# Kernel tuning notes

Hardware: AMD Instinct MI355X
Metric: run time of the kernel (lower is better)

The kernel has to match this reference:

```python
import jax, jax.numpy as jnp
import numpy as np


def setup_inputs() -> dict:
    key = jax.random.key(0)
    k1, k2 = jax.random.split(key)
    latent = jax.random.normal(k1, (131072, 128), dtype=jnp.float32)
    coords = jax.random.normal(k2, (2048, 128), dtype=jnp.float32)
    return {"latent": latent, "coords": coords}


def reference(latent, coords):
    # torch.cdist(latent, coords).min(1)[1]
    # argmin over euclidean distance == argmin over squared distance,
    # so we skip the sqrt (same result, cheaper and numerically safer).
    x2 = jnp.sum(latent * latent, axis=1, keepdims=True)          # [N, 1]
    c2 = jnp.sum(coords * coords, axis=1)                          # [C]
    cross = latent @ coords.T                                      # [N, C]
    d2 = x2 + c2[None, :] - 2.0 * cross                            # [N, C] squared dists
    return jnp.argmin(d2, axis=1)                                  # [N] int indices
```

## Files before the change

kernel.cpp:

```cpp
#include <hip/hip_runtime.h>


constexpr int D = 128;
constexpr int C = 2048;
constexpr int NCH = 32;
constexpr int NCHUNKS = C / NCH;
constexpr int WL_CAP = 32768;

constexpr size_t WS_CNT = 16384;
constexpr size_t WS_WL  = 32768;
constexpr size_t WS_C2F = 196608;
constexpr size_t WS_BH  = 262144;
constexpr size_t WS_BL  = 524288;

typedef __attribute__((ext_vector_type(4))) int i32x4;
typedef unsigned int u32;

__device__ __forceinline__ int pack4(int a0, int a1, int a2, int a3) {
    return (int)(((u32)a0 & 255u) | (((u32)a1 & 255u) << 8) |
                 (((u32)a2 & 255u) << 16) | (((u32)a3 & 255u) << 24));
}

__device__ __forceinline__ void q2(float v, float qa, float inv, float inv128,
                                   int* h, int* l) {
    float hf = __builtin_rintf(v * inv);
    *h = (int)hf;
    float r = fmaf(-hf, qa, v);
    *l = (int)__builtin_rintf(r * inv128);
}

__device__ __forceinline__ void gl_lds16(const void* g, void* l) {
    __builtin_amdgcn_global_load_lds(
        (const __attribute__((address_space(1))) u32*)g,
        (__attribute__((address_space(3))) u32*)l, 16, 0, 0);
}

__global__ __launch_bounds__(1024) void prep_coords(
        const float* __restrict__ coords,
        signed char* __restrict__ Bh,
        signed char* __restrict__ Bl,
        float* __restrict__ c2f, float* __restrict__ qBout,
        int* __restrict__ counter) {
    __shared__ float sW[16];
    int t = blockIdx.x * blockDim.x + threadIdx.x;
    if (t == 0) *counter = 0;

    float m = 0.f;
    for (int i = threadIdx.x; i < C * D / 4; i += 1024) {
        float4 v = ((const float4*)coords)[i];
        m = fmaxf(m, fmaxf(fmaxf(fabsf(v.x), fabsf(v.y)),
                           fmaxf(fabsf(v.z), fabsf(v.w))));
    }
#pragma unroll
    for (int s = 1; s <= 32; s <<= 1) m = fmaxf(m, __shfl_xor(m, s, 64));
    if ((threadIdx.x & 63) == 0) sW[threadIdx.x >> 6] = m;
    __syncthreads();
    float aB = 1e-30f;
#pragma unroll
    for (int i = 0; i < 16; ++i) aB = fmaxf(aB, sW[i]);

    float qb = aB * (1.f / 127.f);
    float inv = 127.f / aB;
    float inv128 = inv * 128.f;
    if (t == 0) *qBout = qb;

    int c = t >> 2, p = t & 3;
    float v[32];
#pragma unroll
    for (int i = 0; i < 8; ++i)
        *(float4*)(v + i * 4) = *(const float4*)(coords + (size_t)c * D + p * 32 + i * 4);
    float ss = 0.f;
#pragma unroll
    for (int j = 0; j < 32; ++j) ss = fmaf(v[j], v[j], ss);
#pragma unroll
    for (int s = 1; s <= 2; s <<= 1) ss += __shfl_xor(ss, s, 64);

#pragma unroll
    for (int g = 0; g < 2; ++g) {
        int g8 = p * 2 + g;
        int hw[4], lw[4];
#pragma unroll
        for (int w = 0; w < 4; ++w) {
            int h0, l0, h1, l1, h2, l2, h3, l3;
            q2(v[g * 16 + w * 4 + 0], qb, inv, inv128, &h0, &l0);
            q2(v[g * 16 + w * 4 + 1], qb, inv, inv128, &h1, &l1);
            q2(v[g * 16 + w * 4 + 2], qb, inv, inv128, &h2, &l2);
            q2(v[g * 16 + w * 4 + 3], qb, inv, inv128, &h3, &l3);
            hw[w] = pack4(h0, h1, h2, h3);
            lw[w] = pack4(l0, l1, l2, l3);
        }
        size_t off = (size_t)c * 128 + (size_t)((g8 ^ (c & 7)) * 16);
        *(i32x4*)(Bh + off) = (i32x4){hw[0], hw[1], hw[2], hw[3]};
        *(i32x4*)(Bl + off) = (i32x4){lw[0], lw[1], lw[2], lw[3]};
    }
    if (p == 0) c2f[c] = -64.f * ss / qb;
}


__global__ __launch_bounds__(256, 2) void centroid_fast(
        const float* __restrict__ latent,
        const signed char* __restrict__ Bh_img,
        const signed char* __restrict__ Bl_img,
        const float* __restrict__ c2f,
        const float* __restrict__ qBp,
        int* __restrict__ out,
        int* __restrict__ counter,
        int* __restrict__ worklist) {
    __shared__ __align__(16) signed char Bh[2][NCH * 128], Bl[2][NCH * 128];

    const int tid  = threadIdx.x;
    const int wid  = tid >> 6;
    const int lane = tid & 63;
    const int q    = lane >> 4, lr = lane & 15;
    const int row_block = blockIdx.x * 128;

    {
        int ph = (blockIdx.x ^ (blockIdx.x >> 8)) & 3;
        for (int i = 0; i < ph * 2; ++i) __builtin_amdgcn_s_sleep(8);
    }

    gl_lds16(Bh_img + tid * 16, &Bh[0][tid * 16]);
    gl_lds16(Bl_img + tid * 16, &Bl[0][tid * 16]);

    const float qB = *qBp;

    i32x4 Ah[2][2], Al[2][2];
    float invqA, qa;
    {
        float v[2][32];
#pragma unroll
        for (int mt = 0; mt < 2; ++mt) {
            const float* rp = latent + (size_t)(row_block + wid * 32 + mt * 16 + lr) * D;
#pragma unroll
            for (int ks = 0; ks < 2; ++ks)
#pragma unroll
                for (int i = 0; i < 4; ++i)
                    *(float4*)(v[mt] + ks * 16 + i * 4) =
                        *(const float4*)(rp + ks * 64 + q * 16 + i * 4);
        }
        float amax = 0.f;
#pragma unroll
        for (int mt = 0; mt < 2; ++mt)
#pragma unroll
            for (int j = 0; j < 32; ++j) amax = fmaxf(amax, fabsf(v[mt][j]));
#pragma unroll
        for (int s = 1; s <= 32; s <<= 1) amax = fmaxf(amax, __shfl_xor(amax, s, 64));
        amax = fmaxf(amax, 1e-30f);
        qa = amax * (1.f / 127.f);
        invqA = 1.f / qa;
        float inv = 127.f / amax;
        float inv128 = inv * 128.f;
#pragma unroll
        for (int mt = 0; mt < 2; ++mt)
#pragma unroll
            for (int ks = 0; ks < 2; ++ks) {
                int hw[4], lw[4];
#pragma unroll
                for (int w = 0; w < 4; ++w) {
                    int h0, l0, h1, l1, h2, l2, h3, l3;
                    q2(v[mt][ks * 16 + w * 4 + 0], qa, inv, inv128, &h0, &l0);
                    q2(v[mt][ks * 16 + w * 4 + 1], qa, inv, inv128, &h1, &l1);
                    q2(v[mt][ks * 16 + w * 4 + 2], qa, inv, inv128, &h2, &l2);
                    q2(v[mt][ks * 16 + w * 4 + 3], qa, inv, inv128, &h3, &l3);
                    hw[w] = pack4(h0, h1, h2, h3);
                    lw[w] = pack4(l0, l1, l2, l3);
                }
                Ah[mt][ks] = (i32x4){hw[0], hw[1], hw[2], hw[3]};
                Al[mt][ks] = (i32x4){lw[0], lw[1], lw[2], lw[3]};
            }
    }
    const int M_int = (int)(1.28f / (qa * qB)) + 1;

    int b1[8], b2[8], bidx[8];
#pragma unroll
    for (int s = 0; s < 8; ++s) {
        b1[s] = -2147483647 - 1; b2[s] = -2147483647 - 1; bidx[s] = 0;
    }

    __syncthreads();

    for (int ch = 0; ch < NCHUNKS; ++ch) {
        const int buf = ch & 1;
        const int chbase = ch * NCH;
        if (ch + 1 < NCHUNKS) {
            const signed char* sh = Bh_img + (size_t)(ch + 1) * (NCH * 128);
            const signed char* sl = Bl_img + (size_t)(ch + 1) * (NCH * 128);
            gl_lds16(sh + tid * 16, &Bh[buf ^ 1][tid * 16]);
            gl_lds16(sl + tid * 16, &Bl[buf ^ 1][tid * 16]);
            asm volatile("s_waitcnt vmcnt(2)" ::: "memory");
        } else {
            asm volatile("s_waitcnt vmcnt(0)" ::: "memory");
        }
        __builtin_amdgcn_s_barrier();

        float cf[2];
        cf[0] = c2f[chbase + lr];
        cf[1] = c2f[chbase + 16 + lr];

#pragma unroll
        for (int nt = 0; nt < 2; ++nt) {
            const int nl = nt * 16 + lr;
            const int v0 = (int)__builtin_rintf(cf[nt] * invqA);
            i32x4 I1[2], I2[2];
#pragma unroll
            for (int mt = 0; mt < 2; ++mt) {
                I1[mt] = (i32x4){0, 0, 0, 0};
                I2[mt] = (i32x4){v0, v0, v0, v0};
            }
            __builtin_amdgcn_s_setprio(1);
#pragma unroll
            for (int ks = 0; ks < 2; ++ks) {
                const int e = nl * 128 + (((ks << 2) | q) ^ (lr & 7)) * 16;
                i32x4 bh = *(const i32x4*)(&Bh[buf][e]);
                i32x4 bl = *(const i32x4*)(&Bl[buf][e]);
#pragma unroll
                for (int mt = 0; mt < 2; ++mt)
                    I1[mt] = __builtin_amdgcn_mfma_i32_16x16x64_i8(Ah[mt][ks], bh, I1[mt], 0, 0, 0);
#pragma unroll
                for (int mt = 0; mt < 2; ++mt)
                    I2[mt] = __builtin_amdgcn_mfma_i32_16x16x64_i8(Ah[mt][ks], bl, I2[mt], 0, 0, 0);
#pragma unroll
                for (int mt = 0; mt < 2; ++mt)
                    I2[mt] = __builtin_amdgcn_mfma_i32_16x16x64_i8(Al[mt][ks], bh, I2[mt], 0, 0, 0);
            }
            __builtin_amdgcn_s_setprio(0);
            const int n_global = chbase + nl;
#pragma unroll
            for (int mt = 0; mt < 2; ++mt)
#pragma unroll
                for (int r = 0; r < 4; ++r) {
                    int slot = mt * 4 + r;
                    int S = (int)(((u32)I1[mt][r] << 7) + (u32)I2[mt][r]);
                    bool gt  = S > b1[slot];
                    b2[slot]   = max(b2[slot], min(S, b1[slot]));
                    b1[slot]   = max(S, b1[slot]);
                    bidx[slot] = gt ? n_global : bidx[slot];
                }
        }
        __builtin_amdgcn_s_barrier();
    }

#pragma unroll
    for (int m = 1; m <= 8; m <<= 1) {
#pragma unroll
        for (int s = 0; s < 8; ++s) {
            int oa = __shfl_xor(b1[s], m, 64);
            int ob = __shfl_xor(b2[s], m, 64);
            int oi = __shfl_xor(bidx[s], m, 64);
            int mn = min(b1[s], oa);
            b2[s] = max(max(b2[s], ob), mn);
            bool take = oa > b1[s];
            b1[s]   = take ? oa : b1[s];
            bidx[s] = take ? oi : bidx[s];
        }
    }
#pragma unroll
    for (int s = 0; s < 8; ++s) {
        if (lr == s) {
            int row = row_block + wid * 32 + (s >> 2) * 16 + q * 4 + (s & 3);
            out[row] = bidx[s];
            if (b1[s] - b2[s] < M_int) {
                int w = atomicAdd(counter, 1);
                if (w < WL_CAP) worklist[w] = row;
            }
        }
    }
}


__global__ __launch_bounds__(1024) void refine_fp64(
        const float* __restrict__ latent, const float* __restrict__ coords,
        const int* __restrict__ worklist, const int* __restrict__ counter,
        int wl_cap, int* __restrict__ out) {
    __shared__ float  xs[D];
    __shared__ double rv[1024];
    __shared__ int    ri[1024];

    int n = *counter;
    if (n > wl_cap) n = wl_cap;

    for (int wi = blockIdx.x; wi < n; wi += gridDim.x) {
        int row = worklist[wi];
        if (threadIdx.x < D)
            xs[threadIdx.x] = latent[(size_t)row * D + threadIdx.x];
        __syncthreads();

        double best = 1.0e300;
        int    bix  = 0;
        for (int c = threadIdx.x; c < C; c += 1024) {
            const float4* cp = (const float4*)(coords + (size_t)c * D);
            double s0 = 0.0, s1 = 0.0, s2 = 0.0, s3 = 0.0;
#pragma unroll 8
            for (int k4 = 0; k4 < 32; ++k4) {
                float4 v = cp[k4];
                double d0 = (double)xs[k4 * 4 + 0] - (double)v.x;
                double d1 = (double)xs[k4 * 4 + 1] - (double)v.y;
                double d2 = (double)xs[k4 * 4 + 2] - (double)v.z;
                double d3 = (double)xs[k4 * 4 + 3] - (double)v.w;
                s0 = fma(d0, d0, s0); s1 = fma(d1, d1, s1);
                s2 = fma(d2, d2, s2); s3 = fma(d3, d3, s3);
            }
            double s = (s0 + s1) + (s2 + s3);
            if (s < best) { best = s; bix = c; }
        }
        rv[threadIdx.x] = best;
        ri[threadIdx.x] = bix;
        __syncthreads();
        for (int off = 512; off > 0; off >>= 1) {
            if (threadIdx.x < off) {
                double ov = rv[threadIdx.x + off];
                int    oi = ri[threadIdx.x + off];
                if (ov < rv[threadIdx.x] ||
                    (ov == rv[threadIdx.x] && oi < ri[threadIdx.x])) {
                    rv[threadIdx.x] = ov;
                    ri[threadIdx.x] = oi;
                }
            }
            __syncthreads();
        }
        if (threadIdx.x == 0) out[row] = ri[0];
        __syncthreads();
    }
}

extern "C" void kernel_launch(void* const* d_in, const int* in_sizes, int n_in,
                              void* d_out, int out_size, void* d_ws, size_t ws_size,
                              hipStream_t stream) {
    const float* latent = (const float*)d_in[0];
    const float* coords = (const float*)d_in[1];
    int*         out    = (int*)d_out;

    char* ws = (char*)d_ws;
    float*  qB      = (float*)ws;
    int*    counter = (int*)(ws + WS_CNT);
    int*    wl      = (int*)(ws + WS_WL);
    float*  c2f     = (float*)(ws + WS_C2F);
    signed char* Bh = (signed char*)(ws + WS_BH);
    signed char* Bl = (signed char*)(ws + WS_BL);
    const int n_rows = in_sizes[0] / D;

    prep_coords<<<8, 1024, 0, stream>>>(coords, Bh, Bl, c2f, qB, counter);
    centroid_fast<<<n_rows / 128, 256, 0, stream>>>(latent, Bh, Bl, c2f, qB, out,
                                                    counter, wl);
    refine_fp64<<<608, 1024, 0, stream>>>(latent, coords, wl, counter, WL_CAP, out);
}
```

Measured before the change: 272.4 us.

## Double chunk size to 64 centroids and software-prefetch B fragments from LDS

Raises the centroid chunk per LDS stage from 32 to 64, halving the number of barrier-separated iterations and doubling the per-thread global-to-LDS copies per stage. It also software-pipelines the LDS reads of B fragments, loading the next k-step or next n-tile's fragments before issuing the current MFMAs. The aim is to hide LDS latency and cut barrier/sync overhead. In exchange it doubles LDS usage per block, which may reduce occupancy, and raises register pressure.

```diff
diff --git a/kernel.cpp b/kernel.cpp
--- a/kernel.cpp
+++ b/kernel.cpp
@@ -3,7 +3,7 @@
 
 constexpr int D = 128;
 constexpr int C = 2048;
-constexpr int NCH = 32;
+constexpr int NCH = 64;
 constexpr int NCHUNKS = C / NCH;
 constexpr int WL_CAP = 32768;
 
@@ -119,8 +119,12 @@
         for (int i = 0; i < ph * 2; ++i) __builtin_amdgcn_s_sleep(8);
     }
 
-    gl_lds16(Bh_img + tid * 16, &Bh[0][tid * 16]);
-    gl_lds16(Bl_img + tid * 16, &Bl[0][tid * 16]);
+#pragma unroll
+    for (int i = 0; i < 2; ++i) {
+        int e = (i * 256 + tid) * 16;
+        gl_lds16(Bh_img + e, &Bh[0][e]);
+        gl_lds16(Bl_img + e, &Bl[0][e]);
+    }
 
     const float qB = *qBp;
 
@@ -185,20 +189,27 @@
         if (ch + 1 < NCHUNKS) {
             const signed char* sh = Bh_img + (size_t)(ch + 1) * (NCH * 128);
             const signed char* sl = Bl_img + (size_t)(ch + 1) * (NCH * 128);
-            gl_lds16(sh + tid * 16, &Bh[buf ^ 1][tid * 16]);
-            gl_lds16(sl + tid * 16, &Bl[buf ^ 1][tid * 16]);
-            asm volatile("s_waitcnt vmcnt(2)" ::: "memory");
+#pragma unroll
+            for (int i = 0; i < 2; ++i) {
+                int e = (i * 256 + tid) * 16;
+                gl_lds16(sh + e, &Bh[buf ^ 1][e]);
+                gl_lds16(sl + e, &Bl[buf ^ 1][e]);
+            }
+            asm volatile("s_waitcnt vmcnt(4)" ::: "memory");
         } else {
             asm volatile("s_waitcnt vmcnt(0)" ::: "memory");
         }
         __builtin_amdgcn_s_barrier();
 
-        float cf[2];
-        cf[0] = c2f[chbase + lr];
-        cf[1] = c2f[chbase + 16 + lr];
-
-#pragma unroll
-        for (int nt = 0; nt < 2; ++nt) {
+        float cf[4];
+#pragma unroll
+        for (int nt = 0; nt < 4; ++nt) cf[nt] = c2f[chbase + nt * 16 + lr];
+
+        i32x4 bh = *(const i32x4*)(&Bh[buf][lr * 128 + (q ^ (lr & 7)) * 16]);
+        i32x4 bl = *(const i32x4*)(&Bl[buf][lr * 128 + (q ^ (lr & 7)) * 16]);
+
+#pragma unroll
+        for (int nt = 0; nt < 4; ++nt) {
             const int nl = nt * 16 + lr;
             const int v0 = (int)__builtin_rintf(cf[nt] * invqA);
             i32x4 I1[2], I2[2];
@@ -210,9 +221,16 @@
             __builtin_amdgcn_s_setprio(1);
 #pragma unroll
             for (int ks = 0; ks < 2; ++ks) {
-                const int e = nl * 128 + (((ks << 2) | q) ^ (lr & 7)) * 16;
-                i32x4 bh = *(const i32x4*)(&Bh[buf][e]);
-                i32x4 bl = *(const i32x4*)(&Bl[buf][e]);
+                i32x4 nbh, nbl;
+                if (ks == 0) {
+                    const int e = nl * 128 + (((1 << 2) | q) ^ (lr & 7)) * 16;
+                    nbh = *(const i32x4*)(&Bh[buf][e]);
+                    nbl = *(const i32x4*)(&Bl[buf][e]);
+                } else if (nt < 3) {
+                    const int e = (nl + 16) * 128 + (q ^ (lr & 7)) * 16;
+                    nbh = *(const i32x4*)(&Bh[buf][e]);
+                    nbl = *(const i32x4*)(&Bl[buf][e]);
+                }
 #pragma unroll
                 for (int mt = 0; mt < 2; ++mt)
                     I1[mt] = __builtin_amdgcn_mfma_i32_16x16x64_i8(Ah[mt][ks], bh, I1[mt], 0, 0, 0);
@@ -222,6 +240,7 @@
 #pragma unroll
                 for (int mt = 0; mt < 2; ++mt)
                     I2[mt] = __builtin_amdgcn_mfma_i32_16x16x64_i8(Al[mt][ks], bh, I2[mt], 0, 0, 0);
+                if (ks == 0 || nt < 3) { bh = nbh; bl = nbl; }
             }
             __builtin_amdgcn_s_setprio(0);
             const int n_global = chbase + nl;
```

New measurement: 271.1 us. Within noise of the previous version (-0.5%).

## Split centroid search into two halves per row block and merge results

Applied to the files above, without the earlier changes.

Each row block is now processed by two workgroups, each scanning half of the centroids and writing its top-two scores and index to a workspace buffer. A new merge kernel combines the two halves, writes the argmin and appends ambiguous rows to the refinement worklist. This doubles the grid to improve load balance and latency hiding. The cost is duplicated latent loading and quantization, an extra kernel launch, and extra global traffic for the partial results.

```diff
diff --git a/kernel.cpp b/kernel.cpp
--- a/kernel.cpp
+++ b/kernel.cpp
@@ -3,8 +3,9 @@
 
 constexpr int D = 128;
 constexpr int C = 2048;
+constexpr int CHALF = 1024;
 constexpr int NCH = 32;
-constexpr int NCHUNKS = C / NCH;
+constexpr int NCHUNKS = CHALF / NCH;
 constexpr int WL_CAP = 32768;
 
 constexpr size_t WS_CNT = 16384;
@@ -12,6 +13,7 @@
 constexpr size_t WS_C2F = 196608;
 constexpr size_t WS_BH  = 262144;
 constexpr size_t WS_BL  = 524288;
+constexpr size_t WS_P   = 786432;
 
 typedef __attribute__((ext_vector_type(4))) int i32x4;
 typedef unsigned int u32;
@@ -103,24 +105,27 @@
         const signed char* __restrict__ Bl_img,
         const float* __restrict__ c2f,
         const float* __restrict__ qBp,
-        int* __restrict__ out,
-        int* __restrict__ counter,
-        int* __restrict__ worklist) {
+        int4* __restrict__ P) {
     __shared__ __align__(16) signed char Bh[2][NCH * 128], Bl[2][NCH * 128];
 
     const int tid  = threadIdx.x;
     const int wid  = tid >> 6;
     const int lane = tid & 63;
     const int q    = lane >> 4, lr = lane & 15;
-    const int row_block = blockIdx.x * 128;
+    const int bid  = blockIdx.x;
+    const int rb   = bid >> 1;
+    const int half = bid & 1;
+    const int row_block = rb * 128;
+    const int cbase0 = half * CHALF;
+    const size_t ibase = (size_t)cbase0 * 128;
 
     {
-        int ph = (blockIdx.x ^ (blockIdx.x >> 8)) & 3;
+        int ph = (bid ^ (bid >> 8)) & 3;
         for (int i = 0; i < ph * 2; ++i) __builtin_amdgcn_s_sleep(8);
     }
 
-    gl_lds16(Bh_img + tid * 16, &Bh[0][tid * 16]);
-    gl_lds16(Bl_img + tid * 16, &Bl[0][tid * 16]);
+    gl_lds16(Bh_img + ibase + tid * 16, &Bh[0][tid * 16]);
+    gl_lds16(Bl_img + ibase + tid * 16, &Bl[0][tid * 16]);
 
     const float qB = *qBp;
 
@@ -181,12 +186,11 @@
 
     for (int ch = 0; ch < NCHUNKS; ++ch) {
         const int buf = ch & 1;
-        const int chbase = ch * NCH;
+        const int chbase = cbase0 + ch * NCH;
         if (ch + 1 < NCHUNKS) {
-            const signed char* sh = Bh_img + (size_t)(ch + 1) * (NCH * 128);
-            const signed char* sl = Bl_img + (size_t)(ch + 1) * (NCH * 128);
-            gl_lds16(sh + tid * 16, &Bh[buf ^ 1][tid * 16]);
-            gl_lds16(sl + tid * 16, &Bl[buf ^ 1][tid * 16]);
+            const size_t off = ibase + (size_t)(ch + 1) * (NCH * 128);
+            gl_lds16(Bh_img + off + tid * 16, &Bh[buf ^ 1][tid * 16]);
+            gl_lds16(Bl_img + off + tid * 16, &Bl[buf ^ 1][tid * 16]);
             asm volatile("s_waitcnt vmcnt(2)" ::: "memory");
         } else {
             asm volatile("s_waitcnt vmcnt(0)" ::: "memory");
@@ -258,12 +262,26 @@
     for (int s = 0; s < 8; ++s) {
         if (lr == s) {
             int row = row_block + wid * 32 + (s >> 2) * 16 + q * 4 + (s & 3);
-            out[row] = bidx[s];
-            if (b1[s] - b2[s] < M_int) {
-                int w = atomicAdd(counter, 1);
-                if (w < WL_CAP) worklist[w] = row;
-            }
-        }
+            P[row * 2 + half] = make_int4(b1[s], b2[s], bidx[s], M_int);
+        }
+    }
+}
+
+
+__global__ __launch_bounds__(256) void merge_halves(
+        const int4* __restrict__ P, int* __restrict__ out,
+        int* __restrict__ counter, int* __restrict__ worklist) {
+    int row = blockIdx.x * 256 + threadIdx.x;
+    int4 a = P[row * 2 + 0];
+    int4 b = P[row * 2 + 1];
+    bool takeB = b.x > a.x;
+    int top = takeB ? b.x : a.x;
+    int idx = takeB ? b.z : a.z;
+    int sec = max(max(a.y, b.y), min(a.x, b.x));
+    out[row] = idx;
+    if (top - sec < a.w) {
+        int w = atomicAdd(counter, 1);
+        if (w < WL_CAP) worklist[w] = row;
     }
 }
 
@@ -337,10 +355,12 @@
     float*  c2f     = (float*)(ws + WS_C2F);
     signed char* Bh = (signed char*)(ws + WS_BH);
     signed char* Bl = (signed char*)(ws + WS_BL);
+    int4*   P       = (int4*)(ws + WS_P);
     const int n_rows = in_sizes[0] / D;
 
     prep_coords<<<8, 1024, 0, stream>>>(coords, Bh, Bl, c2f, qB, counter);
-    centroid_fast<<<n_rows / 128, 256, 0, stream>>>(latent, Bh, Bl, c2f, qB, out,
-                                                    counter, wl);
+    centroid_fast<<<(n_rows / 128) * 2, 256, 0, stream>>>(latent, Bh, Bl, c2f,
+                                                          qB, P);
+    merge_halves<<<n_rows / 256, 256, 0, stream>>>(P, out, counter, wl);
     refine_fp64<<<608, 1024, 0, stream>>>(latent, coords, wl, counter, WL_CAP, out);
 }
```

New measurement: 278.9 us. 2.4% more time.
